# Kernel optimization log

Hardware: AMD Instinct MI355X
Metric: run time of the kernel (lower is better)

Reference implementation:

```python
import jax, jax.numpy as jnp
import numpy as np

N_NODES = 100000
N_USER = 50000
D_IN = 100     # n_units[0]
F_OUT = 16     # n_units[1]
N_HEAD = 3     # n_heads[0]
N_TYPES = 3    # nb_nodes
N_EDGES = 1600000
D2 = 128


def setup_inputs() -> dict:
    key = jax.random.key(0)
    ks = jax.random.split(key, 9)
    h = jax.random.normal(ks[0], (N_NODES, D_IN), dtype=jnp.float32)
    edge_index = jax.random.randint(ks[1], (N_TYPES, 2, N_EDGES), 0, N_NODES, dtype=jnp.int64)
    # per-type GAT params (torch Linear stored transposed: (in, out))
    W = jax.random.normal(ks[2], (N_TYPES, D_IN, N_HEAD * F_OUT), dtype=jnp.float32) * 0.1
    b = jax.random.normal(ks[3], (N_TYPES, N_HEAD * F_OUT), dtype=jnp.float32) * 0.1
    a_src = jax.random.normal(ks[4], (N_TYPES, N_HEAD, F_OUT), dtype=jnp.float32) * 0.1
    a_trg = jax.random.normal(ks[5], (N_TYPES, N_HEAD, F_OUT), dtype=jnp.float32) * 0.1
    # additive attention params
    w1 = jax.random.normal(ks[6], (D_IN, D2), dtype=jnp.float32) * 0.1
    w2 = jax.random.normal(ks[7], (F_OUT, D2), dtype=jnp.float32) * 0.1
    m = jax.random.normal(ks[8], (D2, 1), dtype=jnp.float32) * 0.1
    return {"h": h, "W": W, "b": b, "a_src": a_src, "a_trg": a_trg,
            "w1": w1, "w2": w2, "m": m, "edge_index": edge_index}


def _sparse_gat(h, src, trg, W, b, a_src, a_trg):
    """Single SparseMultiHeadGraphAttention layer followed by head-mean."""
    N = h.shape[0]
    h_prime = (h @ W + b).reshape(N, N_HEAD, F_OUT)  # (N, H, F)
    hs = h_prime[src]                                # (E', H, F) edge gather
    # NOTE: faithful to source — both scores use the src-gathered features
    e = (hs * a_src).sum(-1) + (hs * a_trg).sum(-1)  # (E', H)
    e = jax.nn.leaky_relu(e, negative_slope=0.2)
    e = e - e.max()                                  # global max (as in source)
    exp_e = jnp.exp(e)
    denom = jax.ops.segment_sum(exp_e, trg, num_segments=N)      # (N, H)
    alpha = exp_e / (denom[trg] + 1e-10)                          # (E', H)
    out = jax.ops.segment_sum(hs * alpha[..., None], trg, num_segments=N)  # (N, H, F)
    return out.mean(axis=1)  # == permute(1,0,2).mean(dim=0)


def reference(h, W, b, a_src, a_trg, w1, w2, m, edge_index):
    N = h.shape[0]
    loop = jnp.arange(N, dtype=edge_index.dtype)
    embs = []
    for t in range(N_TYPES):  # small fixed set of relation types
        src = jnp.concatenate([edge_index[t, 0], loop])  # add self-loops
        trg = jnp.concatenate([edge_index[t, 1], loop])
        x = _sparse_gat(h, src, trg, W[t], b[t], a_src[t], a_trg[t])
        embs.append(x[:N_USER])
    type_aware = jnp.stack(embs, axis=1)  # (Nu, |Rs|, F)
    feat = h[:N_USER]                     # (Nu, D)
    # additive attention over types
    q = jnp.tanh((feat @ w1)[:, None, :] + type_aware @ w2)  # (Nu, |Rs|, D2)
    scores = (q @ m)[..., 0]                                  # (Nu, |Rs|)
    beta = jax.nn.softmax(scores, axis=1)
    fusion = jnp.einsum('nr,nrf->nf', beta, type_aware)[:, None, :]  # (Nu,1,F)
    return jnp.concatenate([fusion, type_aware], axis=1)  # (Nu, |Rs|+1, F)
```

## Files before the change

### kernel.cpp

```cpp
#include <hip/hip_runtime.h>
#include <hip/hip_bf16.h>

#define N_NODES 100000
#define N_USER  50000
#define D_IN    100
#define F_OUT   16
#define N_HEAD  3
#define N_TYPES 3
#define N_EDGES 1600000
#define D2      128
#define N_SEG   (N_TYPES * N_USER)
#define KP      136
#define CAP     64
#define CAPH    32
#define NBLK    ((N_NODES + 63) / 64)
#define NPAIR   (N_TYPES * N_EDGES / 2)
#define NBIN    256
#define SEGB    586
#define NBLKA   782
#define PAIRS_A 3072
#define CAPPB   40

typedef __hip_bfloat16 bf16;
typedef __attribute__((ext_vector_type(8))) short bf16x8;
typedef __attribute__((ext_vector_type(4))) float f32x4;
static __device__ __forceinline__ float b2f(bf16 x) { return __bfloat162float(x); }

#define OFF_CVT   64
#define OFF_CW    (OFF_CVT)
#define OFF_CB    (OFF_CW + 14400)
#define OFF_CAS   (OFF_CB + 144)
#define OFF_CAT   (OFF_CAS + 144)
#define OFF_CW1   (OFF_CAT + 144)
#define OFF_CW2   (OFF_CW1 + 12800)
#define OFF_CM    (OFF_CW2 + 2048)
#define CVT_TOTAL 29808
#define OFF_WT    29888
#define OFF_REC   49472
#define OFF_BUCKET OFF_REC
#define OFF_CPB   (OFF_REC + 9600000)
#define OFF_CA    (OFF_CPB + 240000)
#define OFF_CB2   (OFF_CA + 151000)
#define OFF_ELIST (OFF_CB2 + 151000)
#define OFF_TA    (OFF_ELIST + 9600000)
#define OFF_FW1   (OFF_TA + 2400000)

__global__ void k_detect(const unsigned* __restrict__ hraw,
                         const unsigned* __restrict__ eiraw,
                         int* __restrict__ flags) {
    __shared__ int sane, nz;
    if (threadIdx.x == 0) { sane = 0; nz = 0; }
    __syncthreads();
    int cnt = 0; unsigned o = 0;
    for (int i = threadIdx.x; i < 1024; i += 256) {
        unsigned w = hraw[i];
        unsigned e = (w >> 23) & 0xFF;
        if (e >= 64 && e <= 200) cnt++;
        o |= eiraw[2 * i + 1];
    }
    atomicAdd(&sane, cnt);
    atomicOr(&nz, (int)(o != 0));
    __syncthreads();
    if (threadIdx.x == 0) {
        flags[0] = (sane > 512) ? 1 : 0;
        flags[1] = nz ? 0 : 1;
    }
}

__global__ __launch_bounds__(256) void k_convert_w(
        const void* __restrict__ W, const void* __restrict__ b,
        const void* __restrict__ as_, const void* __restrict__ at_,
        const void* __restrict__ w1, const void* __restrict__ w2,
        const void* __restrict__ m, const int* __restrict__ flags,
        float* __restrict__ cvt) {
    int i = blockIdx.x * 256 + threadIdx.x;
    if (i >= CVT_TOTAL) return;
    const void* src; int off;
    if      (i < 14400)                 { src = W;   off = i; }
    else if (i < 14400+144)             { src = b;   off = i - 14400; }
    else if (i < 14400+288)             { src = as_; off = i - 14544; }
    else if (i < 14400+432)             { src = at_; off = i - 14688; }
    else if (i < 14400+432+12800)       { src = w1;  off = i - 14832; }
    else if (i < 14400+432+12800+2048)  { src = w2;  off = i - 27632; }
    else                                { src = m;   off = i - 29680; }
    cvt[i] = flags[0] ? ((const float*)src)[off] : b2f(((const bf16*)src)[off]);
}

__global__ __launch_bounds__(256) void k_make_wt(const void* __restrict__ W,
                                                 const void* __restrict__ w1,
                                                 const int* __restrict__ flags,
                                                 ushort* __restrict__ wt) {
    int i = blockIdx.x * 256 + threadIdx.x;
    if (i >= 6 * 48 * KP) return;
    int g = i / (48 * KP);
    int r = i - g * (48 * KP);
    int n = r / KP, k = r % KP;
    ushort v = 0;
    if (k < D_IN) {
        if (g < 3) {
            size_t src = ((size_t)g * D_IN + k) * 48 + n;
            if (flags[0]) { bf16 x = __float2bfloat16(((const float*)W)[src]); v = *(ushort*)&x; }
            else          { v = ((const ushort*)W)[src]; }
        } else {
            int c = (g - 3) * 48 + n;
            if (c < D2) {
                size_t src = (size_t)k * D2 + c;
                if (flags[0]) { bf16 x = __float2bfloat16(((const float*)w1)[src]); v = *(ushort*)&x; }
                else          { v = ((const ushort*)w1)[src]; }
            }
        }
    }
    wt[i] = v;
}

static __device__ __forceinline__ int2 load_ei2(const void* ei, int f64, size_t pairPos) {
    if (f64) {
        int4 v = ((const int4*)ei)[pairPos];
        int2 r; r.x = v.x; r.y = v.z; return r;
    }
    return ((const int2*)ei)[pairPos];
}

__global__ __launch_bounds__(256) void k_part(const void* __restrict__ ei,
                                              const int* __restrict__ flags,
                                              unsigned* __restrict__ bucket,
                                              unsigned* __restrict__ cpb) {
    __shared__ int bc[NBIN];
    const int f64ei = flags[1];
    const int NE2 = N_EDGES >> 1;
    const int tid = threadIdx.x;
    const int blk = blockIdx.x;
    if (tid < NBIN) bc[tid] = 0;
    __syncthreads();
    const int pair0 = blk * PAIRS_A;
    int npair = NPAIR - pair0; if (npair > PAIRS_A) npair = PAIRS_A;
#pragma unroll
    for (int q = 0; q < PAIRS_A / 256; ++q) {
        int pp = q * 256 + tid;
        int ok = (pp < npair);
        int pg = pair0 + (ok ? pp : 0);
        int t  = (pg >= 2 * NE2) ? 2 : ((pg >= NE2) ? 1 : 0);
        int ep = pg - t * NE2;
        int2 tg = load_ei2(ei, f64ei, (size_t)(t * 2 + 1) * NE2 + ep);
        int2 sr = load_ei2(ei, f64ei, (size_t)(t * 2) * NE2 + ep);
        if (ok && (unsigned)tg.x < N_USER) {
            int seg = t * N_USER + tg.x;
            int bin = seg & 255;
            int pos = atomicAdd(&bc[bin], 1);
            if (pos < CAPPB)
                bucket[((size_t)bin * NBLKA + blk) * CAPPB + pos] =
                    ((unsigned)(seg >> 8) << 17) | (unsigned)sr.x;
        }
        if (ok && (unsigned)tg.y < N_USER) {
            int seg = t * N_USER + tg.y;
            int bin = seg & 255;
            int pos = atomicAdd(&bc[bin], 1);
            if (pos < CAPPB)
                bucket[((size_t)bin * NBLKA + blk) * CAPPB + pos] =
                    ((unsigned)(seg >> 8) << 17) | (unsigned)sr.y;
        }
    }
    __syncthreads();
    if (tid < NBIN) cpb[(size_t)tid * NBLKA + blk] = (unsigned)bc[tid];
}

__global__ __launch_bounds__(256) void k_place(const unsigned* __restrict__ bucket,
                                               const unsigned* __restrict__ cpb,
                                               int* __restrict__ elist,
                                               unsigned* __restrict__ cA,
                                               unsigned* __restrict__ cBv) {
    __shared__ int sc[SEGB];
    const int bin = blockIdx.x >> 1;
    const int h   = blockIdx.x & 1;
    const int tid = threadIdx.x;
    for (int i = tid; i < SEGB; i += 256) sc[i] = 0;
    __syncthreads();
    const int rn = NBLKA / 2;
    for (int j = tid; j < rn; j += 256) {
        int r = 2 * j + h;
        int c = (int)cpb[(size_t)bin * NBLKA + r];
        if (c > CAPPB) c = CAPPB;
        size_t base = ((size_t)bin * NBLKA + r) * CAPPB;
        for (int i4 = 0; i4 < (c + 3) >> 2; ++i4) {
            uint4 wv = *(const uint4*)&bucket[base + 4 * i4];
#pragma unroll
            for (int k = 0; k < 4; ++k) {
                int idx = 4 * i4 + k;
                if (idx < c) {
                    unsigned e = (k == 0) ? wv.x : (k == 1) ? wv.y : (k == 2) ? wv.z : wv.w;
                    int sl  = (int)(e >> 17);
                    int src = (int)(e & 0x1FFFFu);
                    int pos = atomicAdd(&sc[sl], 1);
                    if (pos < CAPH) {
                        size_t seg = ((size_t)sl << 8) + bin;
                        elist[seg * CAP + (h << 5) + pos] = src;
                    }
                }
            }
        }
    }
    __syncthreads();
    for (int s = tid; s < SEGB; s += 256) {
        int seg = (s << 8) + bin;
        if (seg < N_SEG) {
            int cc = sc[s]; if (cc > CAPH) cc = CAPH;
            if (h) cBv[seg] = (unsigned)cc; else cA[seg] = (unsigned)cc;
        }
    }
}

__global__ __launch_bounds__(256) void k_hp_pack(const void* __restrict__ h,
                                                 const ushort* __restrict__ wtg,
                                                 const float* __restrict__ cb,
                                                 const float* __restrict__ cas,
                                                 const float* __restrict__ cat,
                                                 const int* __restrict__ flags,
                                                 float* __restrict__ fw1G,
                                                 float* __restrict__ rec) {
    __shared__ alignas(16) ushort hs[64][KP];
    __shared__ alignas(16) unsigned img[64 * 36];
    const int tid = threadIdx.x;
    const int node0 = blockIdx.x * 64;
    const int f32in = flags[0];
    for (int i = tid; i < 64 * KP; i += 256) {
        int r = i / KP, c = i % KP;
        int n = node0 + r;
        ushort v = 0;
        if (c < D_IN && n < N_NODES) {
            if (f32in) {
                bf16 t16 = __float2bfloat16(((const float*)h)[(size_t)n * D_IN + c]);
                v = *(ushort*)&t16;
            } else {
                v = ((const ushort*)h)[(size_t)n * D_IN + c];
            }
        }
        hs[r][c] = v;
    }
    __syncthreads();
    const int lane = tid & 63;
    const int w    = tid >> 6;
    const int m    = lane & 15;
    const int quad = lane >> 4;
    ushort* img16 = (ushort*)img;
    const int elig = (node0 < N_USER);
    const int nphase = elig ? 6 : 3;
    for (int p = 0; p < nphase; ++p) {
        const ushort* wp = wtg + (size_t)p * 48 * KP;
        f32x4 acc0 = {0.f, 0.f, 0.f, 0.f}, acc1 = acc0, acc2 = acc0;
#pragma unroll
        for (int ks = 0; ks < 4; ++ks) {
            int ko = ks * 32 + quad * 8;
            bf16x8 a  = *(const bf16x8*)&hs[w * 16 + m][ko];
            bf16x8 b0 = *(const bf16x8*)&wp[(0 * 16 + m) * KP + ko];
            bf16x8 b1 = *(const bf16x8*)&wp[(1 * 16 + m) * KP + ko];
            bf16x8 b2 = *(const bf16x8*)&wp[(2 * 16 + m) * KP + ko];
            acc0 = __builtin_amdgcn_mfma_f32_16x16x32_bf16(a, b0, acc0, 0, 0, 0);
            acc1 = __builtin_amdgcn_mfma_f32_16x16x32_bf16(a, b1, acc1, 0, 0, 0);
            acc2 = __builtin_amdgcn_mfma_f32_16x16x32_bf16(a, b2, acc2, 0, 0, 0);
        }
        if (p < 3) {
            const int t = p;
            float hpv[3][4], sred[3][4];
#pragma unroll
            for (int nt = 0; nt < 3; ++nt) {
                int col = nt * 16 + m;
                float bv = cb[t * 48 + col];
                float av = cas[t * 48 + col] + cat[t * 48 + col];
                f32x4 a4 = (nt == 0) ? acc0 : (nt == 1) ? acc1 : acc2;
#pragma unroll
                for (int r = 0; r < 4; ++r) {
                    hpv[nt][r] = a4[r] + bv;
                    sred[nt][r] = hpv[nt][r] * av;
                }
            }
#pragma unroll
            for (int d = 1; d < 16; d <<= 1) {
#pragma unroll
                for (int nt = 0; nt < 3; ++nt)
#pragma unroll
                    for (int r = 0; r < 4; ++r)
                        sred[nt][r] += __shfl_xor(sred[nt][r], d);
            }
            float pk[3][4];
#pragma unroll
            for (int nt = 0; nt < 3; ++nt)
#pragma unroll
                for (int r = 0; r < 4; ++r) {
                    float s = sred[nt][r];
                    s = (s > 0.f) ? s : 0.2f * s;
                    pk[nt][r] = __expf(s);
                }
            __syncthreads();
#pragma unroll
            for (int nt = 0; nt < 3; ++nt) {
                int col = nt * 16 + m;
#pragma unroll
                for (int r = 0; r < 4; ++r) {
                    int row = w * 16 + quad * 4 + r;
                    bf16 gb = __float2bfloat16(pk[nt][r] * hpv[nt][r]);
                    img16[row * 72 + col] = *(ushort*)&gb;
                }
            }
            if (m < 8) {
#pragma unroll
                for (int r = 0; r < 4; ++r) {
                    int row = w * 16 + quad * 4 + r;
                    img[row * 36 + 24 + m] = (m < 3) ? __float_as_uint(pk[m][r]) : 0u;
                }
            }
            __syncthreads();
            {
                int r = tid >> 2, q = tid & 3;
                int n = node0 + r;
                if (n < N_NODES) {
                    const uint4* s = (const uint4*)&img[r * 36 + q * 8];
                    uint4 x0 = s[0], x1 = s[1];
                    uint4* d = (uint4*)((unsigned*)rec + ((size_t)t * N_NODES + n) * 32 + q * 8);
                    d[0] = x0; d[1] = x1;
                }
            }
        } else {
            const int chunk = p - 3;
#pragma unroll
            for (int nt = 0; nt < 3; ++nt) {
                int col = chunk * 48 + nt * 16 + m;
                if (col < D2) {
                    f32x4 a4 = (nt == 0) ? acc0 : (nt == 1) ? acc1 : acc2;
#pragma unroll
                    for (int r = 0; r < 4; ++r) {
                        int row = w * 16 + quad * 4 + r;
                        int v = node0 + row;
                        if (v < N_USER) fw1G[(size_t)v * D2 + col] = a4[r];
                    }
                }
            }
        }
    }
}

__global__ __launch_bounds__(256) void k_gather(const float* __restrict__ rec,
                                                const int* __restrict__ elist,
                                                const unsigned* __restrict__ cA,
                                                const unsigned* __restrict__ cBv,
                                                float* __restrict__ ta) {
    int wid = (blockIdx.x * 256 + threadIdx.x) >> 6;
    if (wid >= N_SEG) return;
    int lane = threadIdx.x & 63;
    int t = wid / N_USER, v = wid - t * N_USER;
    int a = (int)cA[wid];
    int b = (int)cBv[wid];
    int cnt = a + b + 1;
    int b0 = wid * CAP;
    int h = lane >> 5, l = lane & 31;
    const unsigned* recu = (const unsigned*)rec;
    const bool isg = (l < 24);
    const bool isp = (l >= 24) && (l < 27);
    float a0 = 0.f, a1 = 0.f, pacc = 0.f;
    for (int eb = h; eb < cnt; eb += 24) {
        unsigned w[12];
#pragma unroll
        for (int q = 0; q < 12; ++q) {
            int ee = eb + 2 * q;
            w[q] = 0u;
            if (ee < cnt) {
                int src = v;
                if (ee > 0) {
                    int idx  = ee - 1;
                    int slot = (idx < a) ? idx : (32 + idx - a);
                    src = elist[b0 + slot];
                }
                unsigned off = ((unsigned)(t * N_NODES + src) << 5) + l;
                w[q] = recu[off];
            }
        }
#pragma unroll
        for (int q = 0; q < 12; ++q) {
            a0   += isg ? __uint_as_float(w[q] << 16)        : 0.f;
            a1   += isg ? __uint_as_float(w[q] & 0xffff0000u): 0.f;
            pacc += isp ? __uint_as_float(w[q])              : 0.f;
        }
    }
    a0 += __shfl_xor(a0, 32);
    a1 += __shfl_xor(a1, 32);
    pacc += __shfl_xor(pacc, 32);
    int k = (l >> 3); if (k > 2) k = 2;
    float dk = __shfl(pacc, 24 + k) + 1e-10f;
    float r0 = a0 / dk, r1 = a1 / dk;
    float s0 = r0 + __shfl(r0, (l & 7) + 8) + __shfl(r0, (l & 7) + 16);
    float s1 = r1 + __shfl(r1, (l & 7) + 8) + __shfl(r1, (l & 7) + 16);
    if (lane < 8) {
        float2 o;
        o.x = s0 * (1.f / 3.f);
        o.y = s1 * (1.f / 3.f);
        *(float2*)&ta[(size_t)v * 48 + t * 16 + 2 * lane] = o;
    }
}

__global__ __launch_bounds__(256) void k_fuse(const float* __restrict__ fw1G,
                                              const float* __restrict__ cw2,
                                              const float* __restrict__ cm,
                                              const float* __restrict__ ta,
                                              const int* __restrict__ flags,
                                              void* __restrict__ out) {
    __shared__ float w2s[F_OUT * D2];
    __shared__ float ms[D2];
    __shared__ float tas[64][49];
    __shared__ float psum[64][12];
    __shared__ float fus[64][16];
    const int tid = threadIdx.x;
    const int v0 = blockIdx.x * 64;
    const int f32in = flags[0];
    for (int i = tid; i < F_OUT * D2; i += 256) w2s[i] = cw2[i];
    if (tid < D2) ms[tid] = cm[tid];
    {
        int r = tid >> 2, c4 = (tid & 3) * 12;
        int v = v0 + r;
        for (int j = 0; j < 12; ++j)
            tas[r][c4 + j] = (v < N_USER) ? ta[(size_t)v * 48 + c4 + j] : 0.f;
    }
    __syncthreads();
    const int u  = tid & 63;
    const int og = tid >> 6;
    const int v  = v0 + u;
    float tr[48];
#pragma unroll
    for (int x = 0; x < 48; ++x) tr[x] = tas[u][x];
    float acc[2][16];
#pragma unroll
    for (int ph = 0; ph < 2; ++ph) {
        if (v < N_USER) {
            const float4* fr = (const float4*)&fw1G[(size_t)v * D2 + ph * 64 + og * 16];
#pragma unroll
            for (int q = 0; q < 4; ++q) {
                float4 x = fr[q];
                acc[ph][q * 4 + 0] = x.x;
                acc[ph][q * 4 + 1] = x.y;
                acc[ph][q * 4 + 2] = x.z;
                acc[ph][q * 4 + 3] = x.w;
            }
        } else {
#pragma unroll
            for (int j = 0; j < 16; ++j) acc[ph][j] = 0.f;
        }
    }
    float part[3] = {0.f, 0.f, 0.f};
#pragma unroll
    for (int ph = 0; ph < 2; ++ph) {
#pragma unroll
        for (int j = 0; j < 16; ++j) {
            int c = ph * 64 + og * 16 + j;
            float fv = acc[ph][j];
            float mv = ms[c];
#pragma unroll
            for (int t = 0; t < 3; ++t) {
                float z = fv;
#pragma unroll
                for (int f = 0; f < 16; ++f)
                    z += tr[t * 16 + f] * w2s[f * D2 + c];
                float q = 1.f - 2.f / (__expf(2.f * z) + 1.f);
                part[t] += q * mv;
            }
        }
    }
    psum[u][og * 3 + 0] = part[0];
    psum[u][og * 3 + 1] = part[1];
    psum[u][og * 3 + 2] = part[2];
    __syncthreads();
    if (tid < 64) {
        float sc[3];
#pragma unroll
        for (int t = 0; t < 3; ++t)
            sc[t] = psum[tid][t] + psum[tid][3 + t] + psum[tid][6 + t] + psum[tid][9 + t];
        float mx = fmaxf(sc[0], fmaxf(sc[1], sc[2]));
        float e0 = __expf(sc[0] - mx), e1 = __expf(sc[1] - mx), e2 = __expf(sc[2] - mx);
        float inv = 1.f / (e0 + e1 + e2);
#pragma unroll
        for (int f = 0; f < 16; ++f)
            fus[tid][f] = (e0 * tas[tid][f] + e1 * tas[tid][16 + f] + e2 * tas[tid][32 + f]) * inv;
    }
    __syncthreads();
    for (int kq = 0; kq < 16; ++kq) {
        int lin = kq * 256 + tid;
        int r = lin >> 6, c = lin & 63;
        int vv = v0 + r;
        if (vv < N_USER) {
            float val = (c < 16) ? fus[r][c] : tas[r][c - 16];
            size_t oidx = (size_t)vv * 64 + c;
            if (f32in) ((float*)out)[oidx] = val;
            else       ((bf16*)out)[oidx]  = __float2bfloat16(val);
        }
    }
}

extern "C" void kernel_launch(void* const* d_in, const int* in_sizes, int n_in,
                              void* d_out, int out_size, void* d_ws, size_t ws_size,
                              hipStream_t stream) {
    float* ws = (float*)d_ws;
    int*   flags = (int*)ws;
    float* cvt   = ws + OFF_CVT;
    float* cb    = ws + OFF_CB;
    float* cas   = ws + OFF_CAS;
    float* cat   = ws + OFF_CAT;
    float* cw2   = ws + OFF_CW2;
    float* cm    = ws + OFF_CM;
    ushort* wt   = (ushort*)(ws + OFF_WT);
    float* rec   = ws + OFF_REC;
    unsigned* bucket = (unsigned*)(ws + OFF_BUCKET);
    unsigned* cpb    = (unsigned*)(ws + OFF_CPB);
    unsigned* cA     = (unsigned*)(ws + OFF_CA);
    unsigned* cBv    = (unsigned*)(ws + OFF_CB2);
    int*   elist = (int*)(ws + OFF_ELIST);
    float* ta    = ws + OFF_TA;
    float* fw1   = ws + OFF_FW1;

    k_detect<<<1, 256, 0, stream>>>((const unsigned*)d_in[0], (const unsigned*)d_in[8], flags);
    k_convert_w<<<(CVT_TOTAL + 255) / 256, 256, 0, stream>>>(
        d_in[1], d_in[2], d_in[3], d_in[4], d_in[5], d_in[6], d_in[7], flags, cvt);
    k_make_wt<<<(6 * 48 * KP + 255) / 256, 256, 0, stream>>>(d_in[1], d_in[5], flags, wt);

    k_part<<<NBLKA, 256, 0, stream>>>(d_in[8], flags, bucket, cpb);
    k_place<<<NBIN * 2, 256, 0, stream>>>(bucket, cpb, elist, cA, cBv);

    k_hp_pack<<<NBLK, 256, 0, stream>>>(
        d_in[0], wt, cb, cas, cat, flags, fw1, rec);

    k_gather<<<(N_SEG * 64 + 255) / 256, 256, 0, stream>>>(rec, elist, cA, cBv, ta);

    k_fuse<<<(N_USER + 63) / 64, 256, 0, stream>>>(fw1, cw2, cm, ta, flags, d_out);
}
```

Baseline: 428.3 us.

## Merge weight prep kernels and store precomputed byte offsets in edge lists

Folds the two weight-conversion kernels into one launch split by block range, which saves a launch. The placement kernel now writes precomputed byte offsets (type-adjusted node index shifted by 7) into the edge list instead of raw source ids. The gather kernel walks each half-wave's own sub-list directly, drops the per-edge slot and index arithmetic, and handles the self-loop separately. It also merges the denominator accumulation into the a0 accumulator using per-lane masks and shifts, removing one accumulator and one shuffle. The cost is some wasted iterations when the two half-lists differ in length.

```diff
diff --git a/kernel.cpp b/kernel.cpp
--- a/kernel.cpp
+++ b/kernel.cpp
@@ -67,50 +67,49 @@
     }
 }
 
-__global__ __launch_bounds__(256) void k_convert_w(
+#define NBLK_CVT 117
+#define NBLK_WT  153
+__global__ __launch_bounds__(256) void k_prep(
         const void* __restrict__ W, const void* __restrict__ b,
         const void* __restrict__ as_, const void* __restrict__ at_,
         const void* __restrict__ w1, const void* __restrict__ w2,
         const void* __restrict__ m, const int* __restrict__ flags,
-        float* __restrict__ cvt) {
-    int i = blockIdx.x * 256 + threadIdx.x;
-    if (i >= CVT_TOTAL) return;
-    const void* src; int off;
-    if      (i < 14400)                 { src = W;   off = i; }
-    else if (i < 14400+144)             { src = b;   off = i - 14400; }
-    else if (i < 14400+288)             { src = as_; off = i - 14544; }
-    else if (i < 14400+432)             { src = at_; off = i - 14688; }
-    else if (i < 14400+432+12800)       { src = w1;  off = i - 14832; }
-    else if (i < 14400+432+12800+2048)  { src = w2;  off = i - 27632; }
-    else                                { src = m;   off = i - 29680; }
-    cvt[i] = flags[0] ? ((const float*)src)[off] : b2f(((const bf16*)src)[off]);
-}
-
-__global__ __launch_bounds__(256) void k_make_wt(const void* __restrict__ W,
-                                                 const void* __restrict__ w1,
-                                                 const int* __restrict__ flags,
-                                                 ushort* __restrict__ wt) {
-    int i = blockIdx.x * 256 + threadIdx.x;
-    if (i >= 6 * 48 * KP) return;
-    int g = i / (48 * KP);
-    int r = i - g * (48 * KP);
-    int n = r / KP, k = r % KP;
-    ushort v = 0;
-    if (k < D_IN) {
-        if (g < 3) {
-            size_t src = ((size_t)g * D_IN + k) * 48 + n;
-            if (flags[0]) { bf16 x = __float2bfloat16(((const float*)W)[src]); v = *(ushort*)&x; }
-            else          { v = ((const ushort*)W)[src]; }
-        } else {
-            int c = (g - 3) * 48 + n;
-            if (c < D2) {
-                size_t src = (size_t)k * D2 + c;
-                if (flags[0]) { bf16 x = __float2bfloat16(((const float*)w1)[src]); v = *(ushort*)&x; }
-                else          { v = ((const ushort*)w1)[src]; }
-            }
-        }
-    }
-    wt[i] = v;
+        float* __restrict__ cvt, ushort* __restrict__ wt) {
+    if (blockIdx.x < NBLK_CVT) {
+        int i = blockIdx.x * 256 + threadIdx.x;
+        if (i >= CVT_TOTAL) return;
+        const void* src; int off;
+        if      (i < 14400)                 { src = W;   off = i; }
+        else if (i < 14400+144)             { src = b;   off = i - 14400; }
+        else if (i < 14400+288)             { src = as_; off = i - 14544; }
+        else if (i < 14400+432)             { src = at_; off = i - 14688; }
+        else if (i < 14400+432+12800)       { src = w1;  off = i - 14832; }
+        else if (i < 14400+432+12800+2048)  { src = w2;  off = i - 27632; }
+        else                                { src = m;   off = i - 29680; }
+        cvt[i] = flags[0] ? ((const float*)src)[off] : b2f(((const bf16*)src)[off]);
+    } else {
+        int i = (blockIdx.x - NBLK_CVT) * 256 + threadIdx.x;
+        if (i >= 6 * 48 * KP) return;
+        int g = i / (48 * KP);
+        int r = i - g * (48 * KP);
+        int n = r / KP, k = r % KP;
+        ushort v = 0;
+        if (k < D_IN) {
+            if (g < 3) {
+                size_t src = ((size_t)g * D_IN + k) * 48 + n;
+                if (flags[0]) { bf16 x = __float2bfloat16(((const float*)W)[src]); v = *(ushort*)&x; }
+                else          { v = ((const ushort*)W)[src]; }
+            } else {
+                int c = (g - 3) * 48 + n;
+                if (c < D2) {
+                    size_t src = (size_t)k * D2 + c;
+                    if (flags[0]) { bf16 x = __float2bfloat16(((const float*)w1)[src]); v = *(ushort*)&x; }
+                    else          { v = ((const ushort*)w1)[src]; }
+                }
+            }
+        }
+        wt[i] = v;
+    }
 }
 
 static __device__ __forceinline__ int2 load_ei2(const void* ei, int f64, size_t pairPos) {
@@ -192,8 +191,10 @@
                     int src = (int)(e & 0x1FFFFu);
                     int pos = atomicAdd(&sc[sl], 1);
                     if (pos < CAPH) {
-                        size_t seg = ((size_t)sl << 8) + bin;
-                        elist[seg * CAP + (h << 5) + pos] = src;
+                        int seg = (sl << 8) + bin;
+                        int t = seg / N_USER;
+                        elist[(size_t)seg * CAP + (h << 5) + pos] =
+                            (t * N_NODES + src) << 7;
                     }
                 }
             }
@@ -349,49 +350,51 @@
     int t = wid / N_USER, v = wid - t * N_USER;
     int a = (int)cA[wid];
     int b = (int)cBv[wid];
-    int cnt = a + b + 1;
-    int b0 = wid * CAP;
     int h = lane >> 5, l = lane & 31;
-    const unsigned* recu = (const unsigned*)rec;
+    const char* recc = (const char*)rec;
+    const unsigned l4 = (unsigned)(l << 2);
     const bool isg = (l < 24);
-    const bool isp = (l >= 24) && (l < 27);
-    float a0 = 0.f, a1 = 0.f, pacc = 0.f;
-    for (int eb = h; eb < cnt; eb += 24) {
+    const int      s0m = isg ? 16 : 0;
+    const unsigned m0  = isg ? 0xFFFF0000u : 0xFFFFFFFFu;
+    const unsigned m1  = isg ? 0xFFFF0000u : 0u;
+    float a0 = 0.f, a1 = 0.f;
+    if (h == 0) {
+        unsigned off = ((unsigned)(t * N_NODES + v) << 7) + l4;
+        unsigned w = *(const unsigned*)(recc + off);
+        a0 += __uint_as_float((w << s0m) & m0);
+        a1 += __uint_as_float(w & m1);
+    }
+    const int* lst = elist + (size_t)wid * CAP + (h << 5);
+    const int myn = h ? b : a;
+    const int mx = a > b ? a : b;
+    for (int i0 = 0; i0 < mx; i0 += 12) {
         unsigned w[12];
 #pragma unroll
         for (int q = 0; q < 12; ++q) {
-            int ee = eb + 2 * q;
             w[q] = 0u;
-            if (ee < cnt) {
-                int src = v;
-                if (ee > 0) {
-                    int idx  = ee - 1;
-                    int slot = (idx < a) ? idx : (32 + idx - a);
-                    src = elist[b0 + slot];
-                }
-                unsigned off = ((unsigned)(t * N_NODES + src) << 5) + l;
-                w[q] = recu[off];
+            int ee = i0 + q;
+            if (ee < myn) {
+                unsigned off = (unsigned)lst[ee] + l4;
+                w[q] = *(const unsigned*)(recc + off);
             }
         }
 #pragma unroll
         for (int q = 0; q < 12; ++q) {
-            a0   += isg ? __uint_as_float(w[q] << 16)        : 0.f;
-            a1   += isg ? __uint_as_float(w[q] & 0xffff0000u): 0.f;
-            pacc += isp ? __uint_as_float(w[q])              : 0.f;
+            a0 += __uint_as_float((w[q] << s0m) & m0);
+            a1 += __uint_as_float(w[q] & m1);
         }
     }
     a0 += __shfl_xor(a0, 32);
     a1 += __shfl_xor(a1, 32);
-    pacc += __shfl_xor(pacc, 32);
     int k = (l >> 3); if (k > 2) k = 2;
-    float dk = __shfl(pacc, 24 + k) + 1e-10f;
+    float dk = __shfl(a0, 24 + k) + 1e-10f;
     float r0 = a0 / dk, r1 = a1 / dk;
-    float s0 = r0 + __shfl(r0, (l & 7) + 8) + __shfl(r0, (l & 7) + 16);
-    float s1 = r1 + __shfl(r1, (l & 7) + 8) + __shfl(r1, (l & 7) + 16);
+    float sf0 = r0 + __shfl(r0, (l & 7) + 8) + __shfl(r0, (l & 7) + 16);
+    float sf1 = r1 + __shfl(r1, (l & 7) + 8) + __shfl(r1, (l & 7) + 16);
     if (lane < 8) {
         float2 o;
-        o.x = s0 * (1.f / 3.f);
-        o.y = s1 * (1.f / 3.f);
+        o.x = sf0 * (1.f / 3.f);
+        o.y = sf1 * (1.f / 3.f);
         *(float2*)&ta[(size_t)v * 48 + t * 16 + 2 * lane] = o;
     }
 }
@@ -514,9 +517,8 @@
     float* fw1   = ws + OFF_FW1;
 
     k_detect<<<1, 256, 0, stream>>>((const unsigned*)d_in[0], (const unsigned*)d_in[8], flags);
-    k_convert_w<<<(CVT_TOTAL + 255) / 256, 256, 0, stream>>>(
-        d_in[1], d_in[2], d_in[3], d_in[4], d_in[5], d_in[6], d_in[7], flags, cvt);
-    k_make_wt<<<(6 * 48 * KP + 255) / 256, 256, 0, stream>>>(d_in[1], d_in[5], flags, wt);
+    k_prep<<<NBLK_CVT + NBLK_WT, 256, 0, stream>>>(
+        d_in[1], d_in[2], d_in[3], d_in[4], d_in[5], d_in[6], d_in[7], flags, cvt, wt);
 
     k_part<<<NBLKA, 256, 0, stream>>>(d_in[8], flags, bucket, cpb);
     k_place<<<NBIN * 2, 256, 0, stream>>>(bucket, cpb, elist, cA, cBv);
```

Result: no change. 423.3 us (-1.2%).
